# Kernel tuning notes

Hardware: AMD Instinct MI355X
Metric: run time of the kernel (lower is better)

## Reference

```python
import jax, jax.numpy as jnp
import numpy as np

BETA = 0.25
K = 4096


def setup_inputs() -> dict:
    key = jax.random.key(0)
    k1, k2 = jax.random.split(key)
    z = jax.random.normal(k1, (32, 256, 32, 32), dtype=jnp.float32)
    # matches torch init: uniform(-1/k, 1/k)
    embedding = jax.random.uniform(k2, (K, 256), dtype=jnp.float32,
                                   minval=-1.0 / K, maxval=1.0 / K)
    return {"z": z, "embedding": embedding}


def reference(z, embedding):
    b, d, h, w = z.shape
    k = embedding.shape[0]
    # (b d h w) -> (n d)
    z_flat = jnp.transpose(z, (0, 2, 3, 1)).reshape(-1, d)
    # squared euclidean distances, (n, k)
    distances = (jnp.sum(z_flat * z_flat, axis=-1, keepdims=True)
                 + jnp.sum(embedding * embedding, axis=-1)
                 - 2.0 * jnp.einsum('nd,kd->nk', z_flat, embedding))
    encoding_indices = jnp.argmin(distances, axis=1)
    encodings_onehot = jax.nn.one_hot(encoding_indices, k, dtype=z.dtype)
    zq_flat = embedding[encoding_indices]
    z_quantized = jnp.transpose(zq_flat.reshape(b, h, w, d), (0, 3, 1, 2))
    loss_encoder = jnp.mean((jax.lax.stop_gradient(z_quantized) - z) ** 2)
    loss_codebook = jnp.mean((z_quantized - jax.lax.stop_gradient(z)) ** 2)
    loss = BETA * loss_encoder + loss_codebook
    # straight-through estimator
    z_quantized_st = z + jax.lax.stop_gradient(z_quantized - z)
    # perplexity of codebook usage
    enc_mean = jnp.mean(encodings_onehot, axis=0)
    perplexity = jnp.exp(-jnp.sum(enc_mean * jnp.log(enc_mean + 1e-10)))
    return (z_quantized_st, loss, perplexity, encodings_onehot,
            encoding_indices, distances)
```

## Files before the change

### kernel.cpp

```cpp
#include <hip/hip_runtime.h>
#include <hip/hip_bf16.h>

typedef unsigned short u16;
typedef unsigned int u32;
typedef unsigned long long u64;
typedef __attribute__((ext_vector_type(8))) short bf16x8;
typedef __attribute__((ext_vector_type(4))) float f32x4;

#define NROWS 32768
#define KCODES 4096
#define DDIM 256
#define HW 1024
#define ZSTRIDE_B 262144ULL

#define OFF_ZQ   0ULL
#define OFF_LOSS 8388608ULL
#define OFF_PERP 8388609ULL
#define OFF_OH   8388610ULL
#define OFF_IDX  142606338ULL
#define OFF_DIST 142639106ULL

#define T_ZH 16777280ULL
#define T_EH 25165888ULL

#define WS_IDX    0
#define WS_COUNTS 131072
#define WS_EN2    147456
#define WS_ZN2    163840
#define WS_PART   294912
#define WS_BDIST  295424
#define WS_BMIN   524288

__global__ __launch_bounds__(64) void k_prep_e_en2(const float* __restrict__ emb,
                                                   float* __restrict__ en2,
                                                   u16* __restrict__ Ehh) {
    int k = blockIdx.x;
    int l = threadIdx.x;
    float4 v = *(const float4*)(emb + (size_t)k * DDIM + l * 4);
    float s = v.x * v.x + v.y * v.y + v.z * v.z + v.w * v.w;
    #pragma unroll
    for (int m = 32; m; m >>= 1) s += __shfl_xor(s, m);
    if (l == 0) en2[k] = s;
    float vv[4] = {v.x, v.y, v.z, v.w};
    u16 ho[4];
    #pragma unroll
    for (int j = 0; j < 4; ++j) {
        __hip_bfloat16 hb = __float2bfloat16(vv[j]);
        ho[j] = *(u16*)&hb;
    }
    *(ushort4*)(Ehh + (size_t)k * DDIM + l * 4) = make_ushort4(ho[0], ho[1], ho[2], ho[3]);
}

__global__ __launch_bounds__(256) void k_zn2(const float* __restrict__ z,
                                             float* __restrict__ zn2) {
    int n = blockIdx.x * 256 + threadIdx.x;
    int b = n >> 10, hw = n & 1023;
    const float* zp = z + (size_t)b * ZSTRIDE_B + hw;
    float s = 0.f;
    #pragma unroll 8
    for (int d = 0; d < DDIM; ++d) {
        float v = zp[(size_t)d * HW];
        s = fmaf(v, v, s);
    }
    zn2[n] = s;
}

__global__ __launch_bounds__(256) void k_prep_z(const float* __restrict__ z,
                                                u16* __restrict__ Zhh) {
    __shared__ float t[32][132];
    const int tid = threadIdx.x;
    const int h0 = blockIdx.x * 128, d0 = blockIdx.y * 32, b = blockIdx.z;
    const float* zp = z + (size_t)b * ZSTRIDE_B;
    {
        int hq = (tid & 31) << 2;
        int dr = tid >> 5;
        #pragma unroll
        for (int p = 0; p < 4; ++p) {
            int d = p * 8 + dr;
            float4 v = *(const float4*)(zp + (size_t)(d0 + d) * HW + h0 + hq);
            *(float4*)&t[d][hq] = v;
        }
    }
    __syncthreads();
    {
        int nr = tid >> 1;
        int half = tid & 1;
        int n = b * HW + h0 + nr;
        u16 hv[16];
        #pragma unroll
        for (int i = 0; i < 16; ++i) {
            float v = t[half * 16 + i][nr];
            __hip_bfloat16 hb = __float2bfloat16(v);
            hv[i] = *(u16*)&hb;
        }
        u16* dst = Zhh + (size_t)n * DDIM + d0 + half * 16;
        #pragma unroll
        for (int q = 0; q < 4; ++q)
            *(ushort4*)(dst + q * 4) = *(ushort4*)&hv[q * 4];
    }
}

__global__ __launch_bounds__(256) void k_dist_mfma(
    const u16* __restrict__ Zhh, const u16* __restrict__ Ehh,
    const float* __restrict__ zn2, const float* __restrict__ en2,
    float* __restrict__ dist, float* __restrict__ bmin)
{
    __shared__ __align__(16) u16 As[8192];
    __shared__ __align__(16) u16 Bs[8192];
    const int tid = threadIdx.x;
    const int w = tid >> 6, l = tid & 63;
    const int n0 = blockIdx.x * 128, k0 = blockIdx.y * 128;
    const int kb = blockIdx.y;
    const int wr = w >> 1, wc = w & 1;

    int goff[4], loff[4];
    #pragma unroll
    for (int it = 0; it < 4; ++it) {
        int o = (it << 12) + (w << 10) + (l << 4);
        int r = o >> 7;
        int c16 = (o >> 4) & 7;
        int gs = c16 ^ (r & 7);
        goff[it] = r * DDIM + gs * 8;
        loff[it] = (it << 11) + (w << 9);
    }

    f32x4 acc[4][4];
    #pragma unroll
    for (int m = 0; m < 4; ++m)
        #pragma unroll
        for (int n = 0; n < 4; ++n)
            acc[m][n] = (f32x4){0.f, 0.f, 0.f, 0.f};

    const int lr = l & 15, ks = l >> 4;
    const int ra = wr * 64 + lr, rb = wc * 64 + lr;

    const u16* Ap = Zhh + (size_t)n0 * DDIM;
    const u16* Bp = Ehh + (size_t)k0 * DDIM;
    for (int st = 0; st < 4; ++st) {
        const int d0 = st * 64;
        #pragma unroll
        for (int it = 0; it < 4; ++it) {
            __builtin_amdgcn_global_load_lds(
                (const __attribute__((address_space(1))) void*)(Ap + d0 + goff[it]),
                (__attribute__((address_space(3))) void*)(As + loff[it]), 16, 0, 0);
            __builtin_amdgcn_global_load_lds(
                (const __attribute__((address_space(1))) void*)(Bp + d0 + goff[it]),
                (__attribute__((address_space(3))) void*)(Bs + loff[it]), 16, 0, 0);
        }
        __syncthreads();
        #pragma unroll
        for (int kk = 0; kk < 2; ++kk) {
            bf16x8 af[4], bfr[4];
            #pragma unroll
            for (int m = 0; m < 4; ++m) {
                int rr = ra + m * 16;
                af[m] = *(const bf16x8*)&As[rr * 64 + ((kk * 4 + ks) ^ (rr & 7)) * 8];
            }
            #pragma unroll
            for (int n = 0; n < 4; ++n) {
                int rr = rb + n * 16;
                bfr[n] = *(const bf16x8*)&Bs[rr * 64 + ((kk * 4 + ks) ^ (rr & 7)) * 8];
            }
            #pragma unroll
            for (int m = 0; m < 4; ++m)
                #pragma unroll
                for (int n = 0; n < 4; ++n)
                    acc[m][n] = __builtin_amdgcn_mfma_f32_16x16x32_bf16(
                        af[m], bfr[n], acc[m][n], 0, 0, 0);
        }
        __syncthreads();
    }

    float ev[4];
    #pragma unroll
    for (int n = 0; n < 4; ++n) ev[n] = en2[k0 + wc * 64 + n * 16 + lr];
    #pragma unroll
    for (int m = 0; m < 4; ++m) {
        #pragma unroll
        for (int r = 0; r < 4; ++r) {
            int row = n0 + wr * 64 + m * 16 + ks * 4 + r;
            float t = zn2[row];
            float* dp = dist + (size_t)row * KCODES + k0 + wc * 64 + lr;
            float rm = 3.4e38f;
            #pragma unroll
            for (int n = 0; n < 4; ++n) {
                float s  = __fadd_rn(t, ev[n]);
                float m2 = __fmul_rn(2.0f, acc[m][n][r]);
                float dv = __fsub_rn(s, m2);
                dp[n * 16] = dv;
                rm = fminf(rm, dv);
            }
            #pragma unroll
            for (int msk = 1; msk < 16; msk <<= 1)
                rm = fminf(rm, __shfl_xor(rm, msk));
            if (lr == 0)
                bmin[((size_t)row * 32 + kb) * 2 + wc] = rm;
        }
    }
}

__global__ __launch_bounds__(256) void k_select(
    const float* __restrict__ dist, const float* __restrict__ z,
    const float* __restrict__ emb, const float* __restrict__ zn2,
    const float* __restrict__ en2, const float* __restrict__ bmin,
    u32* __restrict__ idxarr, float* __restrict__ bdist)
{
    const int l = threadIdx.x & 63;
    const int row = blockIdx.x * 4 + (threadIdx.x >> 6);
    float bm = bmin[(size_t)row * 64 + l];
    float mn = bm;
    #pragma unroll
    for (int m = 1; m < 64; m <<= 1) mn = fminf(mn, __shfl_xor(mn, m));
    const float thr = mn + 1e-3f;
    u64 qual = __ballot(bm <= thr);

    const int b = row >> 10, hw = row & 1023;
    const float* zp = z + (size_t)b * ZSTRIDE_B + hw;
    float z0 = zp[(size_t)(l * 4 + 0) * HW];
    float z1 = zp[(size_t)(l * 4 + 1) * HW];
    float z2 = zp[(size_t)(l * 4 + 2) * HW];
    float z3 = zp[(size_t)(l * 4 + 3) * HW];
    const float zr = zn2[row];

    u64 best = ~0ull;
    int prev_kb = -1;
    u64 qq = qual;
    while (qq) {
        int bit = __ffsll(qq) - 1; qq &= qq - 1;
        int kb = bit >> 1;
        if (kb == prev_kb) continue;
        prev_kb = kb;
        const float* dr = dist + (size_t)row * KCODES + kb * 128;
        float2 d2 = *(const float2*)(dr + l * 2);
        u64 c0 = __ballot(d2.x <= thr);
        u64 c1 = __ballot(d2.y <= thr);
        u64 any = c0 | c1;
        while (any) {
            int src = __ffsll(any) - 1; any &= any - 1;
            #pragma unroll
            for (int e = 0; e < 2; ++e) {
                u64 msk = e ? c1 : c0;
                if (!((msk >> src) & 1)) continue;
                int k = kb * 128 + src * 2 + e;
                float4 e4 = *(const float4*)(emb + (size_t)k * DDIM + l * 4);
                float p = 0.f;
                p = fmaf(z0, e4.x, p);
                p = fmaf(z1, e4.y, p);
                p = fmaf(z2, e4.z, p);
                p = fmaf(z3, e4.w, p);
                #pragma unroll
                for (int m = 1; m < 64; m <<= 1) p += __shfl_xor(p, m);
                float dh = __fsub_rn(__fadd_rn(zr, en2[k]), __fmul_rn(2.0f, p));
                u32 ub = __float_as_uint(dh);
                ub = (ub & 0x80000000u) ? ~ub : (ub | 0x80000000u);
                u64 cand = ((u64)ub << 32) | (u32)k;
                best = cand < best ? cand : best;
            }
        }
    }
    if (l == 0) {
        idxarr[row] = (u32)(best & 0xffffffffu);
        u32 ub = (u32)(best >> 32);
        u32 fb = (ub & 0x80000000u) ? (ub & 0x7fffffffu) : ~ub;
        bdist[row] = __uint_as_float(fb);
    }
}

__global__ __launch_bounds__(256) void k_zq(const float* __restrict__ emb,
                                            const u32* __restrict__ idxarr,
                                            const float* __restrict__ bdist,
                                            unsigned* __restrict__ counts,
                                            float* __restrict__ out,
                                            float* __restrict__ partials) {
    int n = blockIdx.x * 256 + threadIdx.x;
    unsigned idx = idxarr[n];
    out[OFF_IDX + n] = (float)idx;
    atomicAdd(counts + idx, 1u);
    int b = n >> 10, hw = n & 1023;
    const float* ep = emb + (size_t)idx * DDIM;
    float* oq = out + OFF_ZQ + (size_t)b * ZSTRIDE_B + hw;
    #pragma unroll 4
    for (int d = 0; d < DDIM; ++d)
        oq[(size_t)d * HW] = ep[d];
    __shared__ float red[256];
    red[threadIdx.x] = bdist[n];
    __syncthreads();
    for (int st = 128; st > 0; st >>= 1) {
        if (threadIdx.x < st) red[threadIdx.x] += red[threadIdx.x + st];
        __syncthreads();
    }
    if (threadIdx.x == 0) partials[blockIdx.x] = red[0];
}

__global__ __launch_bounds__(256) void k_onehot(const u32* __restrict__ idxarr,
                                                const unsigned* __restrict__ counts,
                                                const float* __restrict__ partials,
                                                float* __restrict__ out) {
    const int l = threadIdx.x & 63;
    const int n = blockIdx.x * 4 + (threadIdx.x >> 6);
    const int idx = (int)idxarr[n];
    float* base = out + OFF_OH + (size_t)n * KCODES;
    #pragma unroll
    for (int i = 0; i < 16; ++i) {
        int c0 = i * 256 + l * 4;
        float2 a, b2;
        a.x  = (idx == c0)     ? 1.0f : 0.0f;
        a.y  = (idx == c0 + 1) ? 1.0f : 0.0f;
        b2.x = (idx == c0 + 2) ? 1.0f : 0.0f;
        b2.y = (idx == c0 + 3) ? 1.0f : 0.0f;
        *(float2*)(base + c0) = a;
        *(float2*)(base + c0 + 2) = b2;
    }
    if (blockIdx.x == 0) {
        __shared__ float red[256];
        int t = threadIdx.x;
        red[t] = (t < 128) ? partials[t] : 0.f;
        __syncthreads();
        for (int st = 128; st > 0; st >>= 1) {
            if (t < st) red[t] += red[t + st];
            __syncthreads();
        }
        float loss = 1.25f * (red[0] / 8388608.0f);
        __syncthreads();
        float h = 0.f;
        for (int k = t; k < KCODES; k += 256) {
            float p = (float)counts[k] * (1.0f / 32768.0f);
            h -= p * logf(p + 1e-10f);
        }
        red[t] = h;
        __syncthreads();
        for (int st = 128; st > 0; st >>= 1) {
            if (t < st) red[t] += red[t + st];
            __syncthreads();
        }
        if (t == 0) {
            out[OFF_LOSS] = loss;
            out[OFF_PERP] = expf(red[0]);
        }
    }
}

extern "C" void kernel_launch(void* const* d_in, const int* in_sizes, int n_in,
                              void* d_out, int out_size, void* d_ws, size_t ws_size,
                              hipStream_t stream) {
    (void)in_sizes; (void)n_in; (void)out_size; (void)ws_size;
    const float* z = (const float*)d_in[0];
    const float* emb = (const float*)d_in[1];
    float* out = (float*)d_out;
    char* ws = (char*)d_ws;
    u32* idxarr = (u32*)(ws + WS_IDX);
    unsigned* counts = (unsigned*)(ws + WS_COUNTS);
    float* en2 = (float*)(ws + WS_EN2);
    float* zn2 = (float*)(ws + WS_ZN2);
    float* partials = (float*)(ws + WS_PART);
    float* bdist = (float*)(ws + WS_BDIST);
    float* bmin = (float*)(ws + WS_BMIN);

    u16* Zhh = (u16*)(out + T_ZH);
    u16* Ehh = (u16*)(out + T_EH);
    float* dist = out + OFF_DIST;

    hipMemsetAsync(counts, 0, (size_t)KCODES * 4, stream);

    k_prep_z<<<dim3(8, 8, 32), 256, 0, stream>>>(z, Zhh);
    k_prep_e_en2<<<KCODES, 64, 0, stream>>>(emb, en2, Ehh);
    k_zn2<<<NROWS / 256, 256, 0, stream>>>(z, zn2);
    k_dist_mfma<<<dim3(NROWS / 128, KCODES / 128), 256, 0, stream>>>(
        Zhh, Ehh, zn2, en2, dist, bmin);
    k_select<<<NROWS / 4, 256, 0, stream>>>(dist, z, emb, zn2, en2, bmin,
                                            idxarr, bdist);
    k_zq<<<NROWS / 256, 256, 0, stream>>>(emb, idxarr, bdist, counts, out, partials);
    k_onehot<<<NROWS / 4, 256, 0, stream>>>(idxarr, counts, partials, out);
}
```

Before: 566.3 us.

## Fuse zn2 into z prep, stage distance tiles in LDS, use nontemporal stores

Folds the squared-norm computation of z into the bf16 transpose kernel, so z is read once and one launch goes away. The distance epilogue now stages each 16-row slice in shared memory and writes full contiguous rows with nontemporal stores instead of scattered per-lane stores. The zq gather loads the codebook row with float4 and uses nontemporal stores, and the one-hot writer also switches to nontemporal stores. The trade-offs are fewer blocks in prep_z, extra syncthreads in the GEMM epilogue, and the risk that k_select, which reads dist next, no longer finds it in cache.

```diff
diff --git a/kernel.cpp b/kernel.cpp
--- a/kernel.cpp
+++ b/kernel.cpp
@@ -6,6 +6,7 @@
 typedef unsigned long long u64;
 typedef __attribute__((ext_vector_type(8))) short bf16x8;
 typedef __attribute__((ext_vector_type(4))) float f32x4;
+typedef __attribute__((ext_vector_type(2))) float f32x2;
 
 #define NROWS 32768
 #define KCODES 4096
@@ -31,6 +32,14 @@
 #define WS_BDIST  295424
 #define WS_BMIN   524288
 
+static __device__ __forceinline__ void nt_store_f2(float* p, float a, float b) {
+    f32x2 v = {a, b};
+    __builtin_nontemporal_store(v, (f32x2*)p);
+}
+static __device__ __forceinline__ void nt_store_f(float* p, float v) {
+    __builtin_nontemporal_store(v, p);
+}
+
 __global__ __launch_bounds__(64) void k_prep_e_en2(const float* __restrict__ emb,
                                                    float* __restrict__ en2,
                                                    u16* __restrict__ Ehh) {
@@ -51,53 +60,53 @@
     *(ushort4*)(Ehh + (size_t)k * DDIM + l * 4) = make_ushort4(ho[0], ho[1], ho[2], ho[3]);
 }
 
-__global__ __launch_bounds__(256) void k_zn2(const float* __restrict__ z,
-                                             float* __restrict__ zn2) {
-    int n = blockIdx.x * 256 + threadIdx.x;
-    int b = n >> 10, hw = n & 1023;
-    const float* zp = z + (size_t)b * ZSTRIDE_B + hw;
-    float s = 0.f;
-    #pragma unroll 8
-    for (int d = 0; d < DDIM; ++d) {
-        float v = zp[(size_t)d * HW];
-        s = fmaf(v, v, s);
-    }
-    zn2[n] = s;
-}
-
 __global__ __launch_bounds__(256) void k_prep_z(const float* __restrict__ z,
-                                                u16* __restrict__ Zhh) {
+                                                u16* __restrict__ Zhh,
+                                                float* __restrict__ zn2) {
     __shared__ float t[32][132];
     const int tid = threadIdx.x;
-    const int h0 = blockIdx.x * 128, d0 = blockIdx.y * 32, b = blockIdx.z;
+    const int h0 = blockIdx.x * 128, b = blockIdx.y;
     const float* zp = z + (size_t)b * ZSTRIDE_B;
-    {
-        int hq = (tid & 31) << 2;
-        int dr = tid >> 5;
-        #pragma unroll
-        for (int p = 0; p < 4; ++p) {
-            int d = p * 8 + dr;
-            float4 v = *(const float4*)(zp + (size_t)(d0 + d) * HW + h0 + hq);
-            *(float4*)&t[d][hq] = v;
-        }
-    }
-    __syncthreads();
-    {
-        int nr = tid >> 1;
-        int half = tid & 1;
-        int n = b * HW + h0 + nr;
-        u16 hv[16];
-        #pragma unroll
-        for (int i = 0; i < 16; ++i) {
-            float v = t[half * 16 + i][nr];
-            __hip_bfloat16 hb = __float2bfloat16(v);
-            hv[i] = *(u16*)&hb;
-        }
-        u16* dst = Zhh + (size_t)n * DDIM + d0 + half * 16;
-        #pragma unroll
-        for (int q = 0; q < 4; ++q)
-            *(ushort4*)(dst + q * 4) = *(ushort4*)&hv[q * 4];
-    }
+    float zacc = 0.f;
+    for (int slab = 0; slab < 8; ++slab) {
+        const int d0 = slab * 32;
+        __syncthreads();
+        {
+            int hq = (tid & 31) << 2;
+            int dr = tid >> 5;
+            #pragma unroll
+            for (int p = 0; p < 4; ++p) {
+                int d = p * 8 + dr;
+                float4 v = *(const float4*)(zp + (size_t)(d0 + d) * HW + h0 + hq);
+                *(float4*)&t[d][hq] = v;
+            }
+        }
+        __syncthreads();
+        if (tid < 128) {
+            #pragma unroll 8
+            for (int d = 0; d < 32; ++d) {
+                float v = t[d][tid];
+                zacc = fmaf(v, v, zacc);
+            }
+        }
+        {
+            int nr = tid >> 1;
+            int half = tid & 1;
+            int n = b * HW + h0 + nr;
+            u16 hv[16];
+            #pragma unroll
+            for (int i = 0; i < 16; ++i) {
+                float v = t[half * 16 + i][nr];
+                __hip_bfloat16 hb = __float2bfloat16(v);
+                hv[i] = *(u16*)&hb;
+            }
+            u16* dst = Zhh + (size_t)n * DDIM + d0 + half * 16;
+            #pragma unroll
+            for (int q = 0; q < 4; ++q)
+                *(ushort4*)(dst + q * 4) = *(ushort4*)&hv[q * 4];
+        }
+    }
+    if (tid < 128) zn2[b * HW + h0 + tid] = zacc;
 }
 
 __global__ __launch_bounds__(256) void k_dist_mfma(
@@ -105,8 +114,11 @@
     const float* __restrict__ zn2, const float* __restrict__ en2,
     float* __restrict__ dist, float* __restrict__ bmin)
 {
-    __shared__ __align__(16) u16 As[8192];
-    __shared__ __align__(16) u16 Bs[8192];
+    __shared__ __align__(16) u16 smem[17408];
+    u16* As = smem;
+    u16* Bs = smem + 8192;
+    float* Ct = (float*)smem;
+
     const int tid = threadIdx.x;
     const int w = tid >> 6, l = tid & 63;
     const int n0 = blockIdx.x * 128, k0 = blockIdx.y * 128;
@@ -174,20 +186,21 @@
     float ev[4];
     #pragma unroll
     for (int n = 0; n < 4; ++n) ev[n] = en2[k0 + wc * 64 + n * 16 + lr];
+
     #pragma unroll
     for (int m = 0; m < 4; ++m) {
         #pragma unroll
         for (int r = 0; r < 4; ++r) {
             int row = n0 + wr * 64 + m * 16 + ks * 4 + r;
             float t = zn2[row];
-            float* dp = dist + (size_t)row * KCODES + k0 + wc * 64 + lr;
+            int ridx = wr * 16 + ks * 4 + r;
             float rm = 3.4e38f;
             #pragma unroll
             for (int n = 0; n < 4; ++n) {
                 float s  = __fadd_rn(t, ev[n]);
                 float m2 = __fmul_rn(2.0f, acc[m][n][r]);
                 float dv = __fsub_rn(s, m2);
-                dp[n * 16] = dv;
+                Ct[ridx * 132 + wc * 64 + n * 16 + lr] = dv;
                 rm = fminf(rm, dv);
             }
             #pragma unroll
@@ -196,6 +209,16 @@
             if (lr == 0)
                 bmin[((size_t)row * 32 + kb) * 2 + wc] = rm;
         }
+        __syncthreads();
+        #pragma unroll
+        for (int rr = 0; rr < 8; ++rr) {
+            int rid = w * 8 + rr;
+            int grow = n0 + m * 16 + (rid >> 4) * 64 + (rid & 15);
+            float a = Ct[rid * 132 + l * 2];
+            float bvv = Ct[rid * 132 + l * 2 + 1];
+            nt_store_f2(dist + (size_t)grow * KCODES + k0 + l * 2, a, bvv);
+        }
+        __syncthreads();
     }
 }
 
@@ -279,9 +302,14 @@
     int b = n >> 10, hw = n & 1023;
     const float* ep = emb + (size_t)idx * DDIM;
     float* oq = out + OFF_ZQ + (size_t)b * ZSTRIDE_B + hw;
-    #pragma unroll 4
-    for (int d = 0; d < DDIM; ++d)
-        oq[(size_t)d * HW] = ep[d];
+    #pragma unroll 2
+    for (int d = 0; d < DDIM; d += 4) {
+        float4 e4 = *(const float4*)(ep + d);
+        nt_store_f(oq + (size_t)(d + 0) * HW, e4.x);
+        nt_store_f(oq + (size_t)(d + 1) * HW, e4.y);
+        nt_store_f(oq + (size_t)(d + 2) * HW, e4.z);
+        nt_store_f(oq + (size_t)(d + 3) * HW, e4.w);
+    }
     __shared__ float red[256];
     red[threadIdx.x] = bdist[n];
     __syncthreads();
@@ -301,15 +329,14 @@
     const int idx = (int)idxarr[n];
     float* base = out + OFF_OH + (size_t)n * KCODES;
     #pragma unroll
-    for (int i = 0; i < 16; ++i) {
-        int c0 = i * 256 + l * 4;
-        float2 a, b2;
-        a.x  = (idx == c0)     ? 1.0f : 0.0f;
-        a.y  = (idx == c0 + 1) ? 1.0f : 0.0f;
-        b2.x = (idx == c0 + 2) ? 1.0f : 0.0f;
-        b2.y = (idx == c0 + 3) ? 1.0f : 0.0f;
-        *(float2*)(base + c0) = a;
-        *(float2*)(base + c0 + 2) = b2;
+    for (int i = 0; i < 8; ++i) {
+        int c0 = i * 512 + l * 8;
+        #pragma unroll
+        for (int q = 0; q < 4; ++q) {
+            float a = (idx == c0 + 2 * q)     ? 1.0f : 0.0f;
+            float bv = (idx == c0 + 2 * q + 1) ? 1.0f : 0.0f;
+            nt_store_f2(base + c0 + 2 * q, a, bv);
+        }
     }
     if (blockIdx.x == 0) {
         __shared__ float red[256];
@@ -360,11 +387,10 @@
     u16* Ehh = (u16*)(out + T_EH);
     float* dist = out + OFF_DIST;
 
-    hipMemsetAsync(counts, 0, (size_t)KCODES * 4, stream);
-
-    k_prep_z<<<dim3(8, 8, 32), 256, 0, stream>>>(z, Zhh);
+    (void)hipMemsetAsync(counts, 0, (size_t)KCODES * 4, stream);
+
+    k_prep_z<<<dim3(8, 32), 256, 0, stream>>>(z, Zhh, zn2);
     k_prep_e_en2<<<KCODES, 64, 0, stream>>>(emb, en2, Ehh);
-    k_zn2<<<NROWS / 256, 256, 0, stream>>>(z, zn2);
     k_dist_mfma<<<dim3(NROWS / 128, KCODES / 128), 256, 0, stream>>>(
         Zhh, Ehh, zn2, en2, dist, bmin);
     k_select<<<NROWS / 4, 256, 0, stream>>>(dist, z, emb, zn2, en2, bmin,
```

New measurement: 734.0 us. +29.6%, slower.
